# Optimization experiments

Hardware: AMD Instinct MI355X
Metric: run time of the kernel (lower is better)

## Reference

```python
import jax, jax.numpy as jnp
import numpy as np

N_NODES = 100000
N_EDGES = 600000
N_GRAPHS = 1024
F_IN = 32
GHC = 128
NHID = 512
NOUT = 256
N_LAYERS = 5
BN_EPS = 1e-5


def setup_inputs() -> dict:
    key = jax.random.key(0)
    ks = jax.random.split(key, 20)
    x = jax.random.normal(ks[0], (N_NODES, F_IN), dtype=jnp.float32)
    edge_index = jax.random.randint(ks[1], (2, N_EDGES), 0, N_NODES, dtype=jnp.int64)
    batch = jnp.sort(jax.random.randint(ks[2], (N_NODES,), 0, N_GRAPHS, dtype=jnp.int64))
    s = 0.05
    # layer 0 MLP (in=F_IN)
    W1_0 = jax.random.normal(ks[3], (F_IN, 2 * GHC), dtype=jnp.float32) * s
    b1_0 = jnp.zeros((2 * GHC,), jnp.float32)
    W2_0 = jax.random.normal(ks[4], (2 * GHC, GHC), dtype=jnp.float32) * s
    b2_0 = jnp.zeros((GHC,), jnp.float32)
    # layers 1..4 MLPs (in=GHC), stacked
    W1s = jax.random.normal(ks[5], (N_LAYERS - 1, GHC, 2 * GHC), dtype=jnp.float32) * s
    b1s = jnp.zeros((N_LAYERS - 1, 2 * GHC), jnp.float32)
    W2s = jax.random.normal(ks[6], (N_LAYERS - 1, 2 * GHC, GHC), dtype=jnp.float32) * s
    b2s = jnp.zeros((N_LAYERS - 1, GHC), jnp.float32)
    bn_gamma = jnp.ones((N_LAYERS, GHC), jnp.float32)
    bn_beta = jnp.zeros((N_LAYERS, GHC), jnp.float32)
    Wm1 = jax.random.normal(ks[7], (N_LAYERS * GHC, NHID), dtype=jnp.float32) * s
    bm1 = jnp.zeros((NHID,), jnp.float32)
    Wm2 = jax.random.normal(ks[8], (NHID, NOUT), dtype=jnp.float32) * s
    bm2 = jnp.zeros((NOUT,), jnp.float32)
    return dict(x=x, edge_index=edge_index, batch=batch,
                W1_0=W1_0, b1_0=b1_0, W2_0=W2_0, b2_0=b2_0,
                W1s=W1s, b1s=b1s, W2s=W2s, b2s=b2s,
                bn_gamma=bn_gamma, bn_beta=bn_beta,
                Wm1=Wm1, bm1=bm1, Wm2=Wm2, bm2=bm2)


def _gin_layer(x, src, dst, W1, b1, W2, b2, gamma, beta):
    # GINConv (eps=0): h_i = MLP(x_i + sum_{j->i} x_j)
    agg = jax.ops.segment_sum(x[src], dst, num_segments=N_NODES)
    h = x + agg
    h = jax.nn.relu(h @ W1 + b1) @ W2 + b2
    # BatchNorm1d over node dim (training-mode batch stats, biased var)
    mu = jnp.mean(h, axis=0)
    var = jnp.mean(jnp.square(h - mu), axis=0)
    h = (h - mu) * jax.lax.rsqrt(var + BN_EPS) * gamma + beta
    return jax.nn.relu(h)


def _mean_pool(x, batch):
    s = jax.ops.segment_sum(x, batch, num_segments=N_GRAPHS)
    cnt = jax.ops.segment_sum(jnp.ones((x.shape[0],), x.dtype), batch, num_segments=N_GRAPHS)
    return s / jnp.maximum(cnt, 1.0)[:, None]


def reference(x, edge_index, batch, W1_0, b1_0, W2_0, b2_0,
              W1s, b1s, W2s, b2s, bn_gamma, bn_beta, Wm1, bm1, Wm2, bm2):
    src, dst = edge_index[0], edge_index[1]
    xs = []
    h = _gin_layer(x, src, dst, W1_0, b1_0, W2_0, b2_0, bn_gamma[0], bn_beta[0])
    xs.append(_mean_pool(h, batch))
    for l in range(N_LAYERS - 1):  # fixed, structurally distinct params per layer
        h = _gin_layer(h, src, dst, W1s[l], b1s[l], W2s[l], b2s[l],
                       bn_gamma[l + 1], bn_beta[l + 1])
        xs.append(_mean_pool(h, batch))
    z = jnp.concatenate(xs, axis=1)  # [G, 5*GHC]
    z = jax.nn.relu(z @ Wm1 + bm1)
    return z @ Wm2 + bm2  # [G, NOUT]
```

## Files before the change

### kernel.cpp

```cpp
#include <hip/hip_runtime.h>

#define N_NODES 100000
#define N_EDGES 600000
#define N_GRAPHS 1024
#define F_IN 32
#define GHC 128
#define NHID 512
#define NOUT 256
#define N_LAYERS 5
#define BN_EPS 1e-5f

typedef __attribute__((ext_vector_type(4))) float f32x4;
typedef __attribute__((ext_vector_type(8))) short bf16x8;

__device__ __forceinline__ unsigned short f2bf(float f) {
    unsigned int u = __float_as_uint(f);
    u = u + 0x7fffu + ((u >> 16) & 1u);
    return (unsigned short)(u >> 16);
}
__device__ __forceinline__ float bf2f(unsigned short h) {
    return __uint_as_float(((unsigned int)h) << 16);
}
__device__ __forceinline__ void load_lds16(const void* g, void* l) {
    __builtin_amdgcn_global_load_lds((const __attribute__((address_space(1))) void*)g,
                                     (__attribute__((address_space(3))) void*)l, 16, 0, 0);
}

__global__ void deg_kernel(const int* __restrict__ dst, int* __restrict__ deg) {
    int e = blockIdx.x * blockDim.x + threadIdx.x;
    if (e < N_EDGES) atomicAdd(&deg[dst[e]], 1);
}

#define SCHUNK 1024
#define NCHUNKS ((N_NODES + SCHUNK - 1) / SCHUNK)

__global__ __launch_bounds__(1024)
void scan1_kernel(const int* __restrict__ deg, int* __restrict__ ptr, int* __restrict__ btot) {
    __shared__ int buf[SCHUNK];
    int t = threadIdx.x;
    int i = blockIdx.x * SCHUNK + t;
    int v = (i < N_NODES) ? deg[i] : 0;
    buf[t] = v;
    __syncthreads();
    for (int off = 1; off < SCHUNK; off <<= 1) {
        int u = (t >= off) ? buf[t - off] : 0;
        __syncthreads();
        buf[t] += u;
        __syncthreads();
    }
    if (i < N_NODES) ptr[i + 1] = buf[t];
    if (t == SCHUNK - 1) btot[blockIdx.x] = buf[t];
}

__global__ __launch_bounds__(128)
void scan2_kernel(int* __restrict__ btot) {
    __shared__ int buf[128];
    int t = threadIdx.x;
    int v = (t < NCHUNKS) ? btot[t] : 0;
    buf[t] = v;
    __syncthreads();
    for (int off = 1; off < 128; off <<= 1) {
        int u = (t >= off) ? buf[t - off] : 0;
        __syncthreads();
        buf[t] += u;
        __syncthreads();
    }
    if (t < NCHUNKS) btot[t] = buf[t] - v;
}

__global__ void scan3_kernel(int* __restrict__ ptr, const int* __restrict__ btot) {
    int i = blockIdx.x * blockDim.x + threadIdx.x;
    if (i < N_NODES) ptr[i + 1] += btot[i >> 10];
    if (i == 0) ptr[0] = 0;
}

__global__ void fill_kernel(const int* __restrict__ src, const int* __restrict__ dst,
                            int* __restrict__ cur, int* __restrict__ adj) {
    int e = blockIdx.x * blockDim.x + threadIdx.x;
    if (e >= N_EDGES) return;
    int p = atomicAdd(&cur[dst[e]], 1);
    adj[p] = src[e];
}

__global__ void gptr_kernel(const int* __restrict__ batch, int* __restrict__ gptr) {
    int g = blockIdx.x * blockDim.x + threadIdx.x;
    if (g > N_GRAPHS) return;
    int lo = 0, hi = N_NODES;
    while (lo < hi) { int mid = (lo + hi) >> 1; if (batch[mid] < g) lo = mid + 1; else hi = mid; }
    gptr[g] = lo;
}

__global__ void wconv_kernel(const float* __restrict__ W, unsigned short* __restrict__ thi,
                             unsigned short* __restrict__ tlo, int K, int N) {
    int i = blockIdx.x * blockDim.x + threadIdx.x;
    if (i >= K * N) return;
    int k = i / N, n = i - k * N;
    float v = W[i];
    unsigned short h = f2bf(v);
    thi[(size_t)n * K + k] = h;
    tlo[(size_t)n * K + k] = f2bf(v - bf2f(h));
}

template<int F>
__global__ __launch_bounds__(256)
void gather_agg_kernel(const float* __restrict__ x, const int* __restrict__ ptr,
                       const int* __restrict__ adj,
                       unsigned short* __restrict__ ahi, unsigned short* __restrict__ alo) {
    constexpr int F4 = F / 4;
    constexpr int NPB = 256 / F4;
    int f4 = threadIdx.x % F4;
    int n = blockIdx.x * NPB + threadIdx.x / F4;
    if (n >= N_NODES) return;
    const int fo = f4 * 4;
    float4 acc = *(const float4*)(x + (size_t)n * F + fo);
    int p1 = ptr[n + 1];
    for (int p = ptr[n]; p < p1; ++p) {
        int s = adj[p];
        float4 v = *(const float4*)(x + (size_t)s * F + fo);
        acc.x += v.x; acc.y += v.y; acc.z += v.z; acc.w += v.w;
    }
    ushort4 h4, l4;
    h4.x = f2bf(acc.x); l4.x = f2bf(acc.x - bf2f(h4.x));
    h4.y = f2bf(acc.y); l4.y = f2bf(acc.y - bf2f(h4.y));
    h4.z = f2bf(acc.z); l4.z = f2bf(acc.z - bf2f(h4.z));
    h4.w = f2bf(acc.w); l4.w = f2bf(acc.w - bf2f(h4.w));
    *(ushort4*)(ahi + (size_t)n * F + fo) = h4;
    *(ushort4*)(alo + (size_t)n * F + fo) = l4;
}

template<int MODE>
__global__ __launch_bounds__(256)
void mfma_gemm(const unsigned short* __restrict__ Ahi, const unsigned short* __restrict__ Alo,
               const unsigned short* __restrict__ Bhi, const unsigned short* __restrict__ Blo,
               const float* __restrict__ bias,
               unsigned short* __restrict__ Ohi, unsigned short* __restrict__ Olo,
               float* __restrict__ Of, float* __restrict__ bnsums,
               int M, int K, int N)
{
    __shared__ unsigned short As[2][4][128][8];
    __shared__ unsigned short Bs[2][4][128][8];
    __shared__ float sred[128], qred[128];

    const int tid = threadIdx.x;
    const int wv = tid >> 6, lane = tid & 63;
    const int r = lane & 15, g = lane >> 4;
    const int wm = wv >> 1, wn = wv & 1;
    const int row0 = blockIdx.x * 128, col0 = blockIdx.y * 128;

    if (MODE == 2 && tid < 128) { sred[tid] = 0.f; qred[tid] = 0.f; }

    f32x4 acc[4][4];
#pragma unroll
    for (int mi = 0; mi < 4; ++mi)
#pragma unroll
        for (int ni = 0; ni < 4; ++ni) acc[mi][ni] = 0.f;

    for (int k0 = 0; k0 < K; k0 += 32) {
#pragma unroll
        for (int pass = 0; pass < 2; ++pass) {
            const int c = pass * 256 + wv * 64 + lane;
            const int grow = c & 127, gg = c >> 7;
            int arow = row0 + grow; arow = arow < M ? arow : M - 1;
            const size_t aoff = (size_t)arow * K + k0 + gg * 8;
            const size_t boff = (size_t)(col0 + grow) * K + k0 + gg * 8;
            unsigned short* ldsA = (unsigned short*)As + (size_t)(pass * 256 + wv * 64) * 8;
            unsigned short* ldsB = (unsigned short*)Bs + (size_t)(pass * 256 + wv * 64) * 8;
            load_lds16(Ahi + aoff, ldsA);
            load_lds16(Alo + aoff, ldsA + 4096);
            load_lds16(Bhi + boff, ldsB);
            load_lds16(Blo + boff, ldsB + 4096);
        }
        __syncthreads();

        bf16x8 ah[4], al[4], bh[4], bl[4];
#pragma unroll
        for (int i = 0; i < 4; ++i) {
            const int ar = wm * 64 + i * 16 + r;
            const int br = wn * 64 + i * 16 + r;
            ah[i] = *(const bf16x8*)&As[0][g][ar][0];
            al[i] = *(const bf16x8*)&As[1][g][ar][0];
            bh[i] = *(const bf16x8*)&Bs[0][g][br][0];
            bl[i] = *(const bf16x8*)&Bs[1][g][br][0];
        }
#pragma unroll
        for (int mi = 0; mi < 4; ++mi)
#pragma unroll
            for (int ni = 0; ni < 4; ++ni) {
                acc[mi][ni] = __builtin_amdgcn_mfma_f32_16x16x32_bf16(ah[mi], bh[ni], acc[mi][ni], 0, 0, 0);
                acc[mi][ni] = __builtin_amdgcn_mfma_f32_16x16x32_bf16(ah[mi], bl[ni], acc[mi][ni], 0, 0, 0);
                acc[mi][ni] = __builtin_amdgcn_mfma_f32_16x16x32_bf16(al[mi], bh[ni], acc[mi][ni], 0, 0, 0);
            }
        __syncthreads();
    }

    if (MODE == 1) {
#pragma unroll
        for (int ni = 0; ni < 4; ++ni) {
            const int col = col0 + wn * 64 + ni * 16 + r;
            const float bb = bias[col];
#pragma unroll
            for (int mi = 0; mi < 4; ++mi)
#pragma unroll
                for (int reg = 0; reg < 4; ++reg) {
                    const int row = row0 + wm * 64 + mi * 16 + g * 4 + reg;
                    if (row < M) {
                        float v = fmaxf(acc[mi][ni][reg] + bb, 0.f);
                        unsigned short h = f2bf(v);
                        Ohi[(size_t)row * N + col] = h;
                        Olo[(size_t)row * N + col] = f2bf(v - bf2f(h));
                    }
                }
        }
    } else {
        float sl[4] = {0.f, 0.f, 0.f, 0.f}, ql[4] = {0.f, 0.f, 0.f, 0.f};
#pragma unroll
        for (int ni = 0; ni < 4; ++ni) {
            const int col = col0 + wn * 64 + ni * 16 + r;
            const float bb = bias[col];
#pragma unroll
            for (int mi = 0; mi < 4; ++mi)
#pragma unroll
                for (int reg = 0; reg < 4; ++reg) {
                    const int row = row0 + wm * 64 + mi * 16 + g * 4 + reg;
                    if (row < M) {
                        float v = acc[mi][ni][reg] + bb;
                        Of[(size_t)row * N + col] = v;
                        sl[ni] += v; ql[ni] += v * v;
                    }
                }
        }
#pragma unroll
        for (int ni = 0; ni < 4; ++ni) {
            atomicAdd(&sred[wn * 64 + ni * 16 + r], sl[ni]);
            atomicAdd(&qred[wn * 64 + ni * 16 + r], ql[ni]);
        }
        __syncthreads();
        if (tid < 128) {
            atomicAdd(&bnsums[tid], sred[tid]);
            atomicAdd(&bnsums[GHC + tid], qred[tid]);
        }
    }
}

__global__ void bn_finalize_kernel(const float* __restrict__ sums,
    const float* __restrict__ gamma, const float* __restrict__ beta,
    float* __restrict__ ss) {
    int f = threadIdx.x;
    if (f < GHC) {
        float mu = sums[f] * (1.f / N_NODES);
        float var = sums[GHC + f] * (1.f / N_NODES) - mu * mu;
        float sc = gamma[f] * rsqrtf(var + BN_EPS);
        ss[f] = sc;
        ss[GHC + f] = beta[f] - mu * sc;
    }
}

__global__ __launch_bounds__(256)
void bn_apply_kernel(const float* __restrict__ h2, const float* __restrict__ ss,
                     float* __restrict__ hout) {
    int idx = blockIdx.x * blockDim.x + threadIdx.x;
    int node = idx >> 5;
    if (node >= N_NODES) return;
    int f = (idx & 31) * 4;
    float4 v = *(const float4*)(h2 + (size_t)node * GHC + f);
    float4 sc = *(const float4*)(ss + f);
    float4 sh = *(const float4*)(ss + GHC + f);
    float4 o;
    o.x = fmaxf(v.x * sc.x + sh.x, 0.f);
    o.y = fmaxf(v.y * sc.y + sh.y, 0.f);
    o.z = fmaxf(v.z * sc.z + sh.z, 0.f);
    o.w = fmaxf(v.w * sc.w + sh.w, 0.f);
    *(float4*)(hout + (size_t)node * GHC + f) = o;
}

__global__ __launch_bounds__(128)
void pool_kernel(const float* __restrict__ h, const int* __restrict__ gptr,
                 float* __restrict__ z, int loff) {
    int g = blockIdx.x;
    int f = threadIdx.x;
    int s = gptr[g], e = gptr[g + 1];
    float acc = 0.f;
    for (int i = s; i < e; ++i) acc += h[(size_t)i * GHC + f];
    z[(size_t)g * (N_LAYERS * GHC) + loff + f] = acc / fmaxf((float)(e - s), 1.f);
}

template<bool RELU>
__global__ __launch_bounds__(256)
void gemm64_kernel(const float* __restrict__ A, const float* __restrict__ W,
                   const float* __restrict__ bias, float* __restrict__ C,
                   int M, int K, int N) {
    __shared__ float As[16][68];
    __shared__ float Bs[16][64];
    const int tid = threadIdx.x;
    const int row0 = blockIdx.x * 64;
    const int col0 = blockIdx.y * 64;
    const int tx = tid & 15;
    const int ty = tid >> 4;
    const int lm = tid >> 2;
    const int lk = (tid & 3) * 4;
    const int bkr = tid >> 4;
    const int bnc = (tid & 15) * 4;

    float acc[4][4];
#pragma unroll
    for (int i = 0; i < 4; ++i)
#pragma unroll
        for (int j = 0; j < 4; ++j) acc[i][j] = 0.f;

    const int arow = row0 + lm;
    for (int k0 = 0; k0 < K; k0 += 16) {
        if (arow < M) {
            float4 v = *(const float4*)(A + (size_t)arow * K + k0 + lk);
            As[lk + 0][lm] = v.x; As[lk + 1][lm] = v.y;
            As[lk + 2][lm] = v.z; As[lk + 3][lm] = v.w;
        } else {
#pragma unroll
            for (int j = 0; j < 4; ++j) As[lk + j][lm] = 0.f;
        }
        *(float4*)&Bs[bkr][bnc] = *(const float4*)(W + (size_t)(k0 + bkr) * N + col0 + bnc);
        __syncthreads();
#pragma unroll
        for (int kk = 0; kk < 16; ++kk) {
            float a[4], b[4];
            *(float4*)&a[0] = *(const float4*)&As[kk][ty * 4];
            *(float4*)&b[0] = *(const float4*)&Bs[kk][tx * 4];
#pragma unroll
            for (int i = 0; i < 4; ++i)
#pragma unroll
                for (int j = 0; j < 4; ++j)
                    acc[i][j] = fmaf(a[i], b[j], acc[i][j]);
        }
        __syncthreads();
    }
    float4 bv = *(const float4*)(bias + col0 + tx * 4);
    float bb[4] = {bv.x, bv.y, bv.z, bv.w};
#pragma unroll
    for (int i = 0; i < 4; ++i) {
        int row = row0 + ty * 4 + i;
        if (row < M) {
            float o[4];
#pragma unroll
            for (int j = 0; j < 4; ++j) {
                float t = acc[i][j] + bb[j];
                o[j] = RELU ? fmaxf(t, 0.f) : t;
            }
            *(float4*)(C + (size_t)row * N + col0 + tx * 4) = *(float4*)&o[0];
        }
    }
}

extern "C" void kernel_launch(void* const* d_in, const int* in_sizes, int n_in,
                              void* d_out, int out_size, void* d_ws, size_t ws_size,
                              hipStream_t stream)
{
    const float* x = (const float*)d_in[0];
    const int* edge = (const int*)d_in[1];
    const int* batch = (const int*)d_in[2];
    const float* W1_0 = (const float*)d_in[3];
    const float* b1_0 = (const float*)d_in[4];
    const float* W2_0 = (const float*)d_in[5];
    const float* b2_0 = (const float*)d_in[6];
    const float* W1s = (const float*)d_in[7];
    const float* b1s = (const float*)d_in[8];
    const float* W2s = (const float*)d_in[9];
    const float* b2s = (const float*)d_in[10];
    const float* gamma = (const float*)d_in[11];
    const float* beta = (const float*)d_in[12];
    const float* Wm1 = (const float*)d_in[13];
    const float* bm1 = (const float*)d_in[14];
    const float* Wm2 = (const float*)d_in[15];
    const float* bm2 = (const float*)d_in[16];
    const int* srcI = edge;
    const int* dstI = edge + N_EDGES;

    unsigned short* agg_hi = (unsigned short*)d_ws;
    unsigned short* agg_lo = agg_hi + (size_t)N_NODES * GHC;
    float* h2 = (float*)d_ws;
    unsigned short* hid_hi = agg_lo + (size_t)N_NODES * GHC;
    unsigned short* hid_lo = hid_hi + (size_t)N_NODES * 2 * GHC;
    float* hbuf = (float*)(hid_lo + (size_t)N_NODES * 2 * GHC);
    float* z = hbuf + (size_t)N_NODES * GHC;
    float* zh = z + (size_t)N_GRAPHS * N_LAYERS * GHC;
    float* bnsums = zh + (size_t)N_GRAPHS * NHID;
    float* bnss = bnsums + 2 * GHC;
    unsigned short* w1t_hi = (unsigned short*)(bnss + 2 * GHC);
    unsigned short* w1t_lo = w1t_hi + 256 * GHC;
    unsigned short* w2t_hi = w1t_lo + 256 * GHC;
    unsigned short* w2t_lo = w2t_hi + 256 * GHC;
    int* ideg = (int*)(w2t_lo + 256 * GHC);
    int* iptr = ideg + N_NODES;
    int* iadj = iptr + N_NODES + 1;
    int* ibtot = iadj + N_EDGES;
    int* igptr = ibtot + 128;

    hipMemsetAsync(ideg, 0, N_NODES * sizeof(int), stream);
    deg_kernel<<<(N_EDGES + 255) / 256, 256, 0, stream>>>(dstI, ideg);
    scan1_kernel<<<NCHUNKS, SCHUNK, 0, stream>>>(ideg, iptr, ibtot);
    scan2_kernel<<<1, 128, 0, stream>>>(ibtot);
    scan3_kernel<<<(N_NODES + 255) / 256, 256, 0, stream>>>(iptr, ibtot);
    hipMemcpyAsync(ideg, iptr, N_NODES * sizeof(int), hipMemcpyDeviceToDevice, stream);
    fill_kernel<<<(N_EDGES + 255) / 256, 256, 0, stream>>>(srcI, dstI, ideg, iadj);
    gptr_kernel<<<(N_GRAPHS + 1 + 255) / 256, 256, 0, stream>>>(batch, igptr);

    const int MB = (N_NODES + 127) / 128;
    const float* hin = x;
    for (int l = 0; l < N_LAYERS; ++l) {
        const int F = (l == 0) ? F_IN : GHC;
        const float* W1 = (l == 0) ? W1_0 : W1s + (size_t)(l - 1) * GHC * 2 * GHC;
        const float* b1 = (l == 0) ? b1_0 : b1s + (size_t)(l - 1) * 2 * GHC;
        const float* W2 = (l == 0) ? W2_0 : W2s + (size_t)(l - 1) * 2 * GHC * GHC;
        const float* b2 = (l == 0) ? b2_0 : b2s + (size_t)(l - 1) * GHC;

        wconv_kernel<<<(F * 2 * GHC + 255) / 256, 256, 0, stream>>>(W1, w1t_hi, w1t_lo, F, 2 * GHC);
        wconv_kernel<<<(2 * GHC * GHC + 255) / 256, 256, 0, stream>>>(W2, w2t_hi, w2t_lo, 2 * GHC, GHC);

        if (l == 0)
            gather_agg_kernel<F_IN><<<(N_NODES + 31) / 32, 256, 0, stream>>>(hin, iptr, iadj, agg_hi, agg_lo);
        else
            gather_agg_kernel<GHC><<<(N_NODES + 7) / 8, 256, 0, stream>>>(hin, iptr, iadj, agg_hi, agg_lo);

        mfma_gemm<1><<<dim3(MB, 2), 256, 0, stream>>>(agg_hi, agg_lo, w1t_hi, w1t_lo, b1,
                                                      hid_hi, hid_lo, nullptr, nullptr,
                                                      N_NODES, F, 2 * GHC);
        hipMemsetAsync(bnsums, 0, sizeof(float) * 2 * GHC, stream);
        mfma_gemm<2><<<dim3(MB, 1), 256, 0, stream>>>(hid_hi, hid_lo, w2t_hi, w2t_lo, b2,
                                                      nullptr, nullptr, h2, bnsums,
                                                      N_NODES, 2 * GHC, GHC);

        bn_finalize_kernel<<<1, GHC, 0, stream>>>(bnsums, gamma + l * GHC, beta + l * GHC, bnss);
        bn_apply_kernel<<<(N_NODES * 32 + 255) / 256, 256, 0, stream>>>(h2, bnss, hbuf);
        pool_kernel<<<N_GRAPHS, 128, 0, stream>>>(hbuf, igptr, z, l * GHC);

        hin = hbuf;
    }

    dim3 gh1(N_GRAPHS / 64, NHID / 64);
    gemm64_kernel<true><<<gh1, 256, 0, stream>>>(z, Wm1, bm1, zh, N_GRAPHS, N_LAYERS * GHC, NHID);
    dim3 gh2(N_GRAPHS / 64, NOUT / 64);
    gemm64_kernel<false><<<gh2, 256, 0, stream>>>(zh, Wm2, bm2, (float*)d_out, N_GRAPHS, NHID, NOUT);
}
```

Before: 1.584 ms.

## Fuse both GIN MLP GEMMs into one kernel keeping hidden tile in LDS

Replaces the two MFMA GEMM launches per layer with one 512-thread kernel. It computes the 128x256 hidden tile in LDS as a hi/lo bf16 split, then runs the second GEMM with split-K across two wave groups and reduces the partial sums through LDS. Weights are now read straight from global memory instead of being staged in LDS. This removes the 100000x256 hidden-activation round trip to HBM and one launch per layer, at the cost of a large LDS footprint, lower occupancy, and uncached-looking weight loads.

New measurement: 1.476 ms. 1.07x faster.

```diff
diff --git a/kernel.cpp b/kernel.cpp
--- a/kernel.cpp
+++ b/kernel.cpp
@@ -128,59 +128,52 @@
     *(ushort4*)(alo + (size_t)n * F + fo) = l4;
 }
 
-template<int MODE>
-__global__ __launch_bounds__(256)
-void mfma_gemm(const unsigned short* __restrict__ Ahi, const unsigned short* __restrict__ Alo,
-               const unsigned short* __restrict__ Bhi, const unsigned short* __restrict__ Blo,
-               const float* __restrict__ bias,
-               unsigned short* __restrict__ Ohi, unsigned short* __restrict__ Olo,
-               float* __restrict__ Of, float* __restrict__ bnsums,
-               int M, int K, int N)
+__global__ __launch_bounds__(512)
+void fused_mlp_kernel(const unsigned short* __restrict__ Ahi, const unsigned short* __restrict__ Alo,
+                      const unsigned short* __restrict__ W1hi, const unsigned short* __restrict__ W1lo,
+                      const unsigned short* __restrict__ W2hi, const unsigned short* __restrict__ W2lo,
+                      const float* __restrict__ b1, const float* __restrict__ b2,
+                      float* __restrict__ Of, float* __restrict__ bnsums,
+                      int M, int K)
 {
-    __shared__ unsigned short As[2][4][128][8];
-    __shared__ unsigned short Bs[2][4][128][8];
-    __shared__ float sred[128], qred[128];
+    __shared__ __align__(16) unsigned short AsL[2][4][128][8];
+    __shared__ __align__(16) unsigned short hidL[2][32][128][8];
+    __shared__ float sred[GHC], qred[GHC];
 
     const int tid = threadIdx.x;
     const int wv = tid >> 6, lane = tid & 63;
     const int r = lane & 15, g = lane >> 4;
-    const int wm = wv >> 1, wn = wv & 1;
-    const int row0 = blockIdx.x * 128, col0 = blockIdx.y * 128;
-
-    if (MODE == 2 && tid < 128) { sred[tid] = 0.f; qred[tid] = 0.f; }
-
+    const int row0 = blockIdx.x * 128;
+
+    if (tid < GHC) { sred[tid] = 0.f; qred[tid] = 0.f; }
+
+    const int wm = wv >> 2, wn = wv & 3;
     f32x4 acc[4][4];
 #pragma unroll
     for (int mi = 0; mi < 4; ++mi)
 #pragma unroll
         for (int ni = 0; ni < 4; ++ni) acc[mi][ni] = 0.f;
 
+    const int srow = tid & 127, skg = tid >> 7;
+    int arow = row0 + srow; if (arow >= M) arow = M - 1;
+    unsigned short* dA0 = &AsL[0][0][0][0] + wv * 512;
+    unsigned short* dA1 = &AsL[1][0][0][0] + wv * 512;
+
     for (int k0 = 0; k0 < K; k0 += 32) {
-#pragma unroll
-        for (int pass = 0; pass < 2; ++pass) {
-            const int c = pass * 256 + wv * 64 + lane;
-            const int grow = c & 127, gg = c >> 7;
-            int arow = row0 + grow; arow = arow < M ? arow : M - 1;
-            const size_t aoff = (size_t)arow * K + k0 + gg * 8;
-            const size_t boff = (size_t)(col0 + grow) * K + k0 + gg * 8;
-            unsigned short* ldsA = (unsigned short*)As + (size_t)(pass * 256 + wv * 64) * 8;
-            unsigned short* ldsB = (unsigned short*)Bs + (size_t)(pass * 256 + wv * 64) * 8;
-            load_lds16(Ahi + aoff, ldsA);
-            load_lds16(Alo + aoff, ldsA + 4096);
-            load_lds16(Bhi + boff, ldsB);
-            load_lds16(Blo + boff, ldsB + 4096);
-        }
-        __syncthreads();
-
+        const size_t aoff = (size_t)arow * K + k0 + skg * 8;
+        load_lds16(Ahi + aoff, dA0);
+        load_lds16(Alo + aoff, dA1);
+        __syncthreads();
         bf16x8 ah[4], al[4], bh[4], bl[4];
 #pragma unroll
         for (int i = 0; i < 4; ++i) {
             const int ar = wm * 64 + i * 16 + r;
-            const int br = wn * 64 + i * 16 + r;
-            ah[i] = *(const bf16x8*)&As[0][g][ar][0];
-            al[i] = *(const bf16x8*)&As[1][g][ar][0];
-            bh[i] = *(const bf16x8*)&Bs[0][g][br][0];
-            bl[i] = *(const bf16x8*)&Bs[1][g][br][0];
+            ah[i] = *(const bf16x8*)&AsL[0][g][ar][0];
+            al[i] = *(const bf16x8*)&AsL[1][g][ar][0];
+            const int n1 = wn * 64 + i * 16 + r;
+            const size_t w1off = (size_t)n1 * K + k0 + g * 8;
+            bh[i] = *(const bf16x8*)(W1hi + w1off);
+            bl[i] = *(const bf16x8*)(W1lo + w1off);
         }
 #pragma unroll
         for (int mi = 0; mi < 4; ++mi)
@@ -192,53 +185,95 @@
             }
         __syncthreads();
     }
-
-    if (MODE == 1) {
+#pragma unroll
+    for (int ni = 0; ni < 4; ++ni) {
+        const int n1 = wn * 64 + ni * 16 + r;
+        const float bb = b1[n1];
+#pragma unroll
+        for (int mi = 0; mi < 4; ++mi)
+#pragma unroll
+            for (int reg = 0; reg < 4; ++reg) {
+                const int lrow = wm * 64 + mi * 16 + g * 4 + reg;
+                float v = fmaxf(acc[mi][ni][reg] + bb, 0.f);
+                unsigned short h = f2bf(v);
+                hidL[0][n1 >> 3][lrow][n1 & 7] = h;
+                hidL[1][n1 >> 3][lrow][n1 & 7] = f2bf(v - bf2f(h));
+            }
+    }
+    __syncthreads();
+
+    const int wk = wv >> 2, t2 = wv & 3, wm2 = t2 >> 1, wn2 = t2 & 1;
+#pragma unroll
+    for (int mi = 0; mi < 4; ++mi)
+#pragma unroll
+        for (int ni = 0; ni < 4; ++ni) acc[mi][ni] = 0.f;
+
+    const int kb = wk * 128;
+#pragma unroll
+    for (int s = 0; s < 4; ++s) {
+        const int k0 = kb + s * 32;
+        bf16x8 a2h[4], a2l[4], b2h[4], b2l[4];
+#pragma unroll
+        for (int i = 0; i < 4; ++i) {
+            const int ar = wm2 * 64 + i * 16 + r;
+            a2h[i] = *(const bf16x8*)&hidL[0][(k0 >> 3) + g][ar][0];
+            a2l[i] = *(const bf16x8*)&hidL[1][(k0 >> 3) + g][ar][0];
+            const int n2 = wn2 * 64 + i * 16 + r;
+            const size_t w2off = (size_t)n2 * 256 + k0 + g * 8;
+            b2h[i] = *(const bf16x8*)(W2hi + w2off);
+            b2l[i] = *(const bf16x8*)(W2lo + w2off);
+        }
+#pragma unroll
+        for (int mi = 0; mi < 4; ++mi)
+#pragma unroll
+            for (int ni = 0; ni < 4; ++ni) {
+                acc[mi][ni] = __builtin_amdgcn_mfma_f32_16x16x32_bf16(a2h[mi], b2h[ni], acc[mi][ni], 0, 0, 0);
+                acc[mi][ni] = __builtin_amdgcn_mfma_f32_16x16x32_bf16(a2h[mi], b2l[ni], acc[mi][ni], 0, 0, 0);
+                acc[mi][ni] = __builtin_amdgcn_mfma_f32_16x16x32_bf16(a2l[mi], b2h[ni], acc[mi][ni], 0, 0, 0);
+            }
+    }
+    __syncthreads();
+
+    float* scr = (float*)&hidL[0][0][0][0];
+    if (wk == 1) {
+#pragma unroll
+        for (int mi = 0; mi < 4; ++mi)
+#pragma unroll
+            for (int ni = 0; ni < 4; ++ni)
+                *(f32x4*)&scr[((t2 * 64 + ni * 16 + r) * 68 + mi * 16 + g * 4)] = acc[mi][ni];
+    }
+    __syncthreads();
+    if (wk == 0) {
+        float sl[4] = {0.f, 0.f, 0.f, 0.f}, ql[4] = {0.f, 0.f, 0.f, 0.f};
 #pragma unroll
         for (int ni = 0; ni < 4; ++ni) {
-            const int col = col0 + wn * 64 + ni * 16 + r;
-            const float bb = bias[col];
-#pragma unroll
-            for (int mi = 0; mi < 4; ++mi)
+            const int n2 = wn2 * 64 + ni * 16 + r;
+            const float bb = b2[n2];
+#pragma unroll
+            for (int mi = 0; mi < 4; ++mi) {
+                f32x4 p = *(const f32x4*)&scr[((t2 * 64 + ni * 16 + r) * 68 + mi * 16 + g * 4)];
 #pragma unroll
                 for (int reg = 0; reg < 4; ++reg) {
-                    const int row = row0 + wm * 64 + mi * 16 + g * 4 + reg;
-                    if (row < M) {
-                        float v = fmaxf(acc[mi][ni][reg] + bb, 0.f);
-                        unsigned short h = f2bf(v);
-                        Ohi[(size_t)row * N + col] = h;
-                        Olo[(size_t)row * N + col] = f2bf(v - bf2f(h));
-                    }
-                }
-        }
-    } else {
-        float sl[4] = {0.f, 0.f, 0.f, 0.f}, ql[4] = {0.f, 0.f, 0.f, 0.f};
-#pragma unroll
-        for (int ni = 0; ni < 4; ++ni) {
-            const int col = col0 + wn * 64 + ni * 16 + r;
-            const float bb = bias[col];
-#pragma unroll
-            for (int mi = 0; mi < 4; ++mi)
-#pragma unroll
-                for (int reg = 0; reg < 4; ++reg) {
-                    const int row = row0 + wm * 64 + mi * 16 + g * 4 + reg;
-                    if (row < M) {
-                        float v = acc[mi][ni][reg] + bb;
-                        Of[(size_t)row * N + col] = v;
+                    const int grow = row0 + wm2 * 64 + mi * 16 + g * 4 + reg;
+                    if (grow < M) {
+                        float v = acc[mi][ni][reg] + p[reg] + bb;
+                        Of[(size_t)grow * GHC + n2] = v;
                         sl[ni] += v; ql[ni] += v * v;
                     }
                 }
+            }
         }
 #pragma unroll
         for (int ni = 0; ni < 4; ++ni) {
-            atomicAdd(&sred[wn * 64 + ni * 16 + r], sl[ni]);
-            atomicAdd(&qred[wn * 64 + ni * 16 + r], ql[ni]);
-        }
-        __syncthreads();
-        if (tid < 128) {
-            atomicAdd(&bnsums[tid], sred[tid]);
-            atomicAdd(&bnsums[GHC + tid], qred[tid]);
-        }
+            const int n2 = wn2 * 64 + ni * 16 + r;
+            atomicAdd(&sred[n2], sl[ni]);
+            atomicAdd(&qred[n2], ql[ni]);
+        }
+    }
+    __syncthreads();
+    if (tid < GHC) {
+        atomicAdd(&bnsums[tid], sred[tid]);
+        atomicAdd(&bnsums[GHC + tid], qred[tid]);
     }
 }
 
@@ -375,10 +410,8 @@
 
     unsigned short* agg_hi = (unsigned short*)d_ws;
     unsigned short* agg_lo = agg_hi + (size_t)N_NODES * GHC;
-    float* h2 = (float*)d_ws;
-    unsigned short* hid_hi = agg_lo + (size_t)N_NODES * GHC;
-    unsigned short* hid_lo = hid_hi + (size_t)N_NODES * 2 * GHC;
-    float* hbuf = (float*)(hid_lo + (size_t)N_NODES * 2 * GHC);
+    float* h2 = (float*)(agg_lo + (size_t)N_NODES * GHC);
+    float* hbuf = h2 + (size_t)N_NODES * GHC;
     float* z = hbuf + (size_t)N_NODES * GHC;
     float* zh = z + (size_t)N_GRAPHS * N_LAYERS * GHC;
     float* bnsums = zh + (size_t)N_GRAPHS * NHID;
@@ -419,13 +452,9 @@
         else
             gather_agg_kernel<GHC><<<(N_NODES + 7) / 8, 256, 0, stream>>>(hin, iptr, iadj, agg_hi, agg_lo);
 
-        mfma_gemm<1><<<dim3(MB, 2), 256, 0, stream>>>(agg_hi, agg_lo, w1t_hi, w1t_lo, b1,
-                                                      hid_hi, hid_lo, nullptr, nullptr,
-                                                      N_NODES, F, 2 * GHC);
         hipMemsetAsync(bnsums, 0, sizeof(float) * 2 * GHC, stream);
-        mfma_gemm<2><<<dim3(MB, 1), 256, 0, stream>>>(hid_hi, hid_lo, w2t_hi, w2t_lo, b2,
-                                                      nullptr, nullptr, h2, bnsums,
-                                                      N_NODES, 2 * GHC, GHC);
+        fused_mlp_kernel<<<MB, 512, 0, stream>>>(agg_hi, agg_lo, w1t_hi, w1t_lo, w2t_hi, w2t_lo,
+                                                 b1, b2, h2, bnsums, N_NODES, F);
 
         bn_finalize_kernel<<<1, GHC, 0, stream>>>(bnsums, gamma + l * GHC, beta + l * GHC, bnss);
         bn_apply_kernel<<<(N_NODES * 32 + 255) / 256, 256, 0, stream>>>(h2, bnss, hbuf);
```
